# Performance work log

Measured on AMD Instinct MI355X. Metric: run time of the kernel, lower is better.

Reference implementation:

```python
import jax, jax.numpy as jnp
import numpy as np

B, T, D = 2, 2048, 1024
H, K = 16, 64  # num_heads, key_size (value_size == key_size)


def setup_inputs() -> dict:
    key = jax.random.key(0)
    ks = jax.random.split(key, 9)
    # xavier-uniform-ish scale for square-ish projections
    def xavier(k, shape):
        fan_in, fan_out = shape[0], shape[1]
        lim = jnp.sqrt(6.0 / (fan_in + fan_out))
        return jax.random.uniform(k, shape, jnp.float32, -lim, lim)
    return {
        "x_q": jax.random.normal(ks[0], (B, T, D), jnp.float32),
        "Wq": xavier(ks[1], (D, H * K)),
        "bq": jnp.zeros((H * K,), jnp.float32),
        "Wk": xavier(ks[2], (D, H * K)),
        "bk": jnp.zeros((H * K,), jnp.float32),
        "Wv": xavier(ks[3], (D, H * K)),
        "bv": jnp.zeros((H * K,), jnp.float32),
        "Wo": xavier(ks[4], (H * K, D)),
        "bo": jnp.zeros((D,), jnp.float32),
    }


def reference(x_q, Wq, bq, Wk, bk, Wv, bv, Wo, bo):
    # self-attention: x_k = x_v = x_q
    q = (x_q @ Wq + bq).reshape(B, T, H, K)
    k = (x_q @ Wk + bk).reshape(B, T, H, K)
    v = (x_q @ Wv + bv).reshape(B, T, H, K)
    # dense_dot_product_attention, mask=None
    logits = jnp.einsum('bqhd,bkhd->bhqk', q, k) / jnp.sqrt(jnp.asarray(K, k.dtype))
    attn_w = jax.nn.softmax(logits, axis=-1)  # [B,H,Tq,Tk]
    attn = jnp.einsum('bhqk,bkhd->bqhd', attn_w, v).reshape(B, T, H * K)
    out = attn @ Wo + bo  # [B,T,D]
    return out
```

## Files before the change

### kernel.cpp

```cpp
#include <hip/hip_runtime.h>
#include <hip/hip_bf16.h>
#include <stdint.h>

#define B_  2
#define T_  2048
#define D_  1024
#define H_  16
#define KS  64
#define M_  (B_*T_)

typedef unsigned short u16;
typedef __bf16 bf16x8 __attribute__((ext_vector_type(8)));
typedef __bf16 bf16x4 __attribute__((ext_vector_type(4)));
typedef float  f32x4  __attribute__((ext_vector_type(4)));

#define AS1 __attribute__((address_space(1)))
#define AS3 __attribute__((address_space(3)))

__device__ inline u16 f2bf(float x){
  union { float f; uint32_t u; } v; v.f = x;
  uint32_t r = (v.u + 0x7fffu + ((v.u >> 16) & 1u)) >> 16;
  return (u16)r;
}

__device__ inline void gl_lds16(const u16* g, u16* l){
  __builtin_amdgcn_global_load_lds((AS1 void*)(const_cast<u16*>(g)),
                                   (AS3 void*)l, 16, 0, 0);
}

__global__ __launch_bounds__(256) void k_cvt_x(const float* __restrict__ x,
                                               u16* __restrict__ xb){
  int i = blockIdx.x * 256 + threadIdx.x;
  float4 v = ((const float4*)x)[i];
  ushort4 o;
  o.x = f2bf(v.x); o.y = f2bf(v.y); o.z = f2bf(v.z); o.w = f2bf(v.w);
  ((ushort4*)xb)[i] = o;
}

__global__ __launch_bounds__(256) void k_tconv_w(const float* __restrict__ W0,
                                                 const float* __restrict__ W1,
                                                 const float* __restrict__ W2,
                                                 const float* __restrict__ W3,
                                                 u16* __restrict__ out){
  const float* W = (blockIdx.z==0)?W0:(blockIdx.z==1)?W1:(blockIdx.z==2)?W2:W3;
  u16* o = out + (size_t)blockIdx.z * 1024 * 1024;
  __shared__ float tile[32][33];
  int tx = threadIdx.x, ty = threadIdx.y;
  int kb = blockIdx.y * 32, nb = blockIdx.x * 32;
  for(int i=0;i<4;i++) tile[ty+8*i][tx] = W[(size_t)(kb+ty+8*i)*1024 + nb+tx];
  __syncthreads();
  for(int i=0;i<4;i++){
    int n = nb + ty + 8*i;
    o[(size_t)n*1024 + kb + tx] = f2bf(tile[tx][ty+8*i]);
  }
}

__global__ __launch_bounds__(256) void k_gemm_qkv(const u16* __restrict__ xb,
                                                  const u16* __restrict__ wt,
                                                  const float* __restrict__ bq,
                                                  const float* __restrict__ bk,
                                                  const float* __restrict__ bv,
                                                  u16* __restrict__ qkv){
  int widx = blockIdx.x >> 3;
  int n0   = (blockIdx.x & 7) * 128;
  int m0   = blockIdx.y * 128;
  const u16* BT = wt + (size_t)widx * (1024*1024);
  const float* bias = (widx==0)?bq:(widx==1)?bk:bv;
  u16* out = qkv + (size_t)widx * (4*1024*1024);
  float oscale = (widx==0) ? 0.125f * 1.44269504088896f : 1.0f;

  __shared__ u16 Asm[128*64];
  __shared__ u16 Bsm[128*64];
  int t = threadIdx.x;
  int lane = t & 63, w = t >> 6, wm = w >> 1, wn = w & 1;
  int l15 = lane & 15, l4 = lane >> 4;
  f32x4 zero = {0.f,0.f,0.f,0.f};
  f32x4 acc[4][4];
  for(int i=0;i<4;i++) for(int j=0;j<4;j++) acc[i][j] = zero;
  int srow = t >> 3, schunk = t & 7;

  for(int kt=0; kt<16; ++kt){
    __syncthreads();
    int kb = kt * 64;
    for(int i=0;i<4;i++){
      int row = i*32 + srow;
      int gch = schunk ^ (row & 7);
      gl_lds16(xb + (size_t)(m0+row)*1024 + kb + gch*8, Asm + row*64 + schunk*8);
      gl_lds16(BT + (size_t)(n0+row)*1024 + kb + gch*8, Bsm + row*64 + schunk*8);
    }
    __syncthreads();
    for(int c=0;c<2;c++){
      bf16x8 af[4], bfr[4];
      for(int mt=0;mt<4;mt++){
        int row = wm*64 + mt*16 + l15;
        int idx = (row*64 + c*32 + l4*8) ^ ((row & 7) << 3);
        af[mt] = *(const bf16x8*)(Asm + idx);
      }
      for(int nt=0;nt<4;nt++){
        int row = wn*64 + nt*16 + l15;
        int idx = (row*64 + c*32 + l4*8) ^ ((row & 7) << 3);
        bfr[nt] = *(const bf16x8*)(Bsm + idx);
      }
      for(int mt=0;mt<4;mt++)
        for(int nt=0;nt<4;nt++)
          acc[mt][nt] = __builtin_amdgcn_mfma_f32_16x16x32_bf16(af[mt], bfr[nt], acc[mt][nt], 0,0,0);
    }
  }
  for(int nt=0;nt<4;nt++){
    int nbase = n0 + wn*64 + nt*16 + l15;
    float bv_ = bias[nbase];
    int h = nbase >> 6, kk = nbase & 63;
    for(int mt=0;mt<4;mt++){
      for(int r=0;r<4;r++){
        int m = m0 + wm*64 + mt*16 + l4*4 + r;
        int b = m >> 11, tt = m & 2047;
        out[(((size_t)(b*H_ + h)*T_ + tt) << 6) + kk] = f2bf((acc[mt][nt][r] + bv_) * oscale);
      }
    }
  }
}

__global__ __launch_bounds__(256) void k_tpose_v(const u16* __restrict__ V,
                                                 u16* __restrict__ VT){
  __shared__ u16 tile[64][65];
  int bh = blockIdx.y, tt = blockIdx.x;
  const u16* v = V + ((size_t)bh*T_ + (size_t)tt*64) * 64;
  u16* o = VT + (size_t)bh*64*T_ + (size_t)tt*64;
  int t = threadIdx.x;
  for(int i=0;i<2;i++){
    int r = i*32 + (t>>3); int c0 = (t&7)*8;
    bf16x8 d = *(const bf16x8*)(v + (size_t)r*64 + c0);
    for(int j=0;j<8;j++) tile[r][c0+j] = ((u16*)&d)[j];
  }
  __syncthreads();
  for(int i=0;i<2;i++){
    int d0 = i*32 + (t>>3); int c0 = (t&7)*8;
    union { u16 s[8]; uint4 q; } pk;
    for(int j=0;j<8;j++) pk.s[j] = tile[c0+j][d0];
    *(uint4*)(o + (size_t)d0*T_ + c0) = pk.q;
  }
}

__global__ __launch_bounds__(256) void k_attn(const u16* __restrict__ Q,
                                              const u16* __restrict__ Kg,
                                              const u16* __restrict__ VT,
                                              u16* __restrict__ attn_out){
  int bx = blockIdx.x;
  int qt = bx & 31, h = (bx >> 5) & 15, b = bx >> 9;
  int bh = b*H_ + h;
  const u16* Qh = Q  + (size_t)bh * T_ * 64;
  const u16* Kh = Kg + (size_t)bh * T_ * 64;
  const u16* Vh = VT + (size_t)bh * 64 * T_;
  __shared__ u16 Ksm[2][64*64];
  __shared__ u16 Vsm[2][64*64];
  __shared__ u16 Psm[4][16*64];
  int t = threadIdx.x, lane = t & 63, w = t >> 6;
  int l15 = lane & 15, l4 = lane >> 4;

  bf16x8 qf[2];
  int qrow = qt*64 + w*16 + l15;
  for(int c=0;c<2;c++)
    qf[c] = *(const bf16x8*)(Qh + (size_t)qrow*64 + c*32 + l4*8);

  f32x4 zero = {0.f,0.f,0.f,0.f};
  f32x4 accT[4];
  for(int g=0;g<4;g++) accT[g] = zero;
  float m_r = -3.0e38f, l_r = 0.f;

  int srow = t >> 3, schunk = t & 7;

  for(int i=0;i<2;i++){
    int row = i*32 + srow;
    int gch = schunk ^ (row & 7);
    gl_lds16(Kh + (size_t)row*64 + gch*8,  &Ksm[0][row*64 + schunk*8]);
    gl_lds16(Vh + (size_t)row*T_ + gch*8,  &Vsm[0][row*64 + schunk*8]);
  }
  __syncthreads();

  int cur = 0;
  for(int tile=0; tile<32; ++tile){
    if(tile+1 < 32){
      int kvb = (tile+1)*64;
      for(int i=0;i<2;i++){
        int row = i*32 + srow;
        int gch = schunk ^ (row & 7);
        gl_lds16(Kh + (size_t)(kvb+row)*64 + gch*8, &Ksm[cur^1][row*64 + schunk*8]);
        gl_lds16(Vh + (size_t)row*T_ + kvb + gch*8, &Vsm[cur^1][row*64 + schunk*8]);
      }
    }

    f32x4 s[4];
    for(int g=0;g<4;g++) s[g] = zero;
    for(int c=0;c<2;c++){
      for(int g=0;g<4;g++){
        int row = g*16 + l15;
        int idx = (row*64 + c*32 + l4*8) ^ ((row & 7) << 3);
        bf16x8 kf = *(const bf16x8*)(&Ksm[cur][idx]);
        s[g] = __builtin_amdgcn_mfma_f32_16x16x32_bf16(kf, qf[c], s[g], 0,0,0);
      }
    }

    float pmax = s[0][0];
    for(int g=0;g<4;g++)
      for(int r=0;r<4;r++) pmax = fmaxf(pmax, s[g][r]);
    pmax = fmaxf(pmax, __shfl_xor(pmax, 16));
    pmax = fmaxf(pmax, __shfl_xor(pmax, 32));
    float mnew  = fmaxf(m_r, pmax);
    float alpha = __builtin_amdgcn_exp2f(m_r - mnew);
    m_r = mnew;
    float rs = 0.f;
    for(int g=0;g<4;g++)
      for(int r=0;r<4;r++){
        float e = __builtin_amdgcn_exp2f(s[g][r] - mnew);
        s[g][r] = e;
        rs += e;
      }
    rs += __shfl_xor(rs, 16);
    rs += __shfl_xor(rs, 32);
    l_r = l_r * alpha + rs;
    for(int g=0;g<4;g++){
      f32x4 a = accT[g];
      for(int r=0;r<4;r++) a[r] *= alpha;
      accT[g] = a;
    }

    for(int g=0;g<4;g++){
      bf16x4 pk;
      for(int r=0;r<4;r++) pk[r] = (__bf16)s[g][r];
      int idx = (l15*64 + g*16 + l4*4) ^ ((l15 & 7) << 3);
      *(bf16x4*)(&Psm[w][idx]) = pk;
    }

    for(int c=0;c<2;c++){
      int idx_p = (l15*64 + c*32 + l4*8) ^ ((l15 & 7) << 3);
      bf16x8 pf = *(const bf16x8*)(&Psm[w][idx_p]);
      for(int g=0;g<4;g++){
        int row = g*16 + l15;
        int idx = (row*64 + c*32 + l4*8) ^ ((row & 7) << 3);
        bf16x8 vf = *(const bf16x8*)(&Vsm[cur][idx]);
        accT[g] = __builtin_amdgcn_mfma_f32_16x16x32_bf16(vf, pf, accT[g], 0,0,0);
      }
    }

    __syncthreads();
    cur ^= 1;
  }

  float oinv = 1.0f / l_r;
  int m = b*T_ + qt*64 + w*16 + l15;
  for(int g=0;g<4;g++){
    bf16x4 pk;
    for(int r=0;r<4;r++) pk[r] = (__bf16)(accT[g][r] * oinv);
    *(bf16x4*)(attn_out + (size_t)m*1024 + h*64 + g*16 + l4*4) = pk;
  }
}

__global__ __launch_bounds__(256) void k_gemm_out(const u16* __restrict__ A,
                                                  const u16* __restrict__ BT,
                                                  const float* __restrict__ bias,
                                                  float* __restrict__ out){
  int n0 = blockIdx.x * 128;
  int m0 = blockIdx.y * 128;
  __shared__ u16 Asm[128*64];
  __shared__ u16 Bsm[128*64];
  int t = threadIdx.x;
  int lane = t & 63, w = t >> 6, wm = w >> 1, wn = w & 1;
  int l15 = lane & 15, l4 = lane >> 4;
  f32x4 zero = {0.f,0.f,0.f,0.f};
  f32x4 acc[4][4];
  for(int i=0;i<4;i++) for(int j=0;j<4;j++) acc[i][j] = zero;
  int srow = t >> 3, schunk = t & 7;

  for(int kt=0; kt<16; ++kt){
    __syncthreads();
    int kb = kt * 64;
    for(int i=0;i<4;i++){
      int row = i*32 + srow;
      int gch = schunk ^ (row & 7);
      gl_lds16(A  + (size_t)(m0+row)*1024 + kb + gch*8, Asm + row*64 + schunk*8);
      gl_lds16(BT + (size_t)(n0+row)*1024 + kb + gch*8, Bsm + row*64 + schunk*8);
    }
    __syncthreads();
    for(int c=0;c<2;c++){
      bf16x8 af[4], bfr[4];
      for(int mt=0;mt<4;mt++){
        int row = wm*64 + mt*16 + l15;
        int idx = (row*64 + c*32 + l4*8) ^ ((row & 7) << 3);
        af[mt] = *(const bf16x8*)(Asm + idx);
      }
      for(int nt=0;nt<4;nt++){
        int row = wn*64 + nt*16 + l15;
        int idx = (row*64 + c*32 + l4*8) ^ ((row & 7) << 3);
        bfr[nt] = *(const bf16x8*)(Bsm + idx);
      }
      for(int mt=0;mt<4;mt++)
        for(int nt=0;nt<4;nt++)
          acc[mt][nt] = __builtin_amdgcn_mfma_f32_16x16x32_bf16(af[mt], bfr[nt], acc[mt][nt], 0,0,0);
    }
  }
  for(int nt=0;nt<4;nt++){
    int nbase = n0 + wn*64 + nt*16 + l15;
    float bv_ = bias[nbase];
    for(int mt=0;mt<4;mt++){
      for(int r=0;r<4;r++){
        int m = m0 + wm*64 + mt*16 + l4*4 + r;
        out[(size_t)m*1024 + nbase] = acc[mt][nt][r] + bv_;
      }
    }
  }
}

extern "C" void kernel_launch(void* const* d_in, const int* in_sizes, int n_in,
                              void* d_out, int out_size, void* d_ws, size_t ws_size,
                              hipStream_t stream){
  const float* x  = (const float*)d_in[0];
  const float* Wq = (const float*)d_in[1];
  const float* bq = (const float*)d_in[2];
  const float* Wk = (const float*)d_in[3];
  const float* bk = (const float*)d_in[4];
  const float* Wv = (const float*)d_in[5];
  const float* bv = (const float*)d_in[6];
  const float* Wo = (const float*)d_in[7];
  const float* bo = (const float*)d_in[8];
  float* out = (float*)d_out;
  char* ws = (char*)d_ws;

  u16* xb  = (u16*)(ws);
  u16* wt  = (u16*)(ws + (8u  << 20));
  u16* qkv = (u16*)(ws + (16u << 20));
  u16* vt  = (u16*)(ws + (40u << 20));
  u16* at  = (u16*)(ws + (48u << 20));

  k_cvt_x   <<<4096, 256, 0, stream>>>(x, xb);
  k_tconv_w <<<dim3(32,32,4), dim3(32,8), 0, stream>>>(Wq, Wk, Wv, Wo, wt);
  k_gemm_qkv<<<dim3(24,32), 256, 0, stream>>>(xb, wt, bq, bk, bv, qkv);
  k_tpose_v <<<dim3(32,32), 256, 0, stream>>>(qkv + (size_t)8*1024*1024, vt);
  k_attn    <<<1024, 256, 0, stream>>>(qkv, qkv + (size_t)4*1024*1024, vt, at);
  k_gemm_out<<<dim3(8,32), 256, 0, stream>>>(at, wt + (size_t)3*1024*1024, bo, out);
}
```

Measured before the change: 228.3 us.

## Load V directly to registers, lazily rescale softmax, raise MFMA priority, shrink out-GEMM tile

The attention kernel now reads V fragments straight from global memory into registers each tile instead of staging them through double-buffered shared memory. It also skips the online-softmax rescale unless the running max grows by more than a threshold, and raises wave priority around the MFMA blocks. The output GEMM tile drops from 128x128 to 64x128, doubling the grid for better CU occupancy. Direct V loads are issued in the same iteration they are used, so their latency may be exposed, and the lazy rescale risks exp overflow if logits are large.

```diff
diff --git a/kernel.cpp b/kernel.cpp
--- a/kernel.cpp
+++ b/kernel.cpp
@@ -152,7 +152,6 @@
   const u16* Kh = Kg + (size_t)bh * T_ * 64;
   const u16* Vh = VT + (size_t)bh * 64 * T_;
   __shared__ u16 Ksm[2][64*64];
-  __shared__ u16 Vsm[2][64*64];
   __shared__ u16 Psm[4][16*64];
   int t = threadIdx.x, lane = t & 63, w = t >> 6;
   int l15 = lane & 15, l4 = lane >> 4;
@@ -172,25 +171,31 @@
   for(int i=0;i<2;i++){
     int row = i*32 + srow;
     int gch = schunk ^ (row & 7);
-    gl_lds16(Kh + (size_t)row*64 + gch*8,  &Ksm[0][row*64 + schunk*8]);
-    gl_lds16(Vh + (size_t)row*T_ + gch*8,  &Vsm[0][row*64 + schunk*8]);
+    gl_lds16(Kh + (size_t)row*64 + gch*8, &Ksm[0][row*64 + schunk*8]);
   }
   __syncthreads();
 
   int cur = 0;
   for(int tile=0; tile<32; ++tile){
+    int kv0 = tile*64;
+
+    bf16x8 vf[2][4];
+    for(int c=0;c<2;c++)
+      for(int g=0;g<4;g++)
+        vf[c][g] = *(const bf16x8*)(Vh + (size_t)(g*16+l15)*T_ + kv0 + c*32 + l4*8);
+
     if(tile+1 < 32){
-      int kvb = (tile+1)*64;
+      int kvb = kv0 + 64;
       for(int i=0;i<2;i++){
         int row = i*32 + srow;
         int gch = schunk ^ (row & 7);
         gl_lds16(Kh + (size_t)(kvb+row)*64 + gch*8, &Ksm[cur^1][row*64 + schunk*8]);
-        gl_lds16(Vh + (size_t)row*T_ + kvb + gch*8, &Vsm[cur^1][row*64 + schunk*8]);
       }
     }
 
     f32x4 s[4];
     for(int g=0;g<4;g++) s[g] = zero;
+    __builtin_amdgcn_s_setprio(1);
     for(int c=0;c<2;c++){
       for(int g=0;g<4;g++){
         int row = g*16 + l15;
@@ -199,30 +204,34 @@
         s[g] = __builtin_amdgcn_mfma_f32_16x16x32_bf16(kf, qf[c], s[g], 0,0,0);
       }
     }
+    __builtin_amdgcn_s_setprio(0);
 
     float pmax = s[0][0];
     for(int g=0;g<4;g++)
       for(int r=0;r<4;r++) pmax = fmaxf(pmax, s[g][r]);
     pmax = fmaxf(pmax, __shfl_xor(pmax, 16));
     pmax = fmaxf(pmax, __shfl_xor(pmax, 32));
-    float mnew  = fmaxf(m_r, pmax);
-    float alpha = __builtin_amdgcn_exp2f(m_r - mnew);
-    m_r = mnew;
+    if(__any(pmax > m_r + 8.f)){
+      float mnew  = fmaxf(m_r, pmax);
+      float alpha = __builtin_amdgcn_exp2f(m_r - mnew);
+      m_r = mnew;
+      l_r *= alpha;
+      for(int g=0;g<4;g++){
+        f32x4 a = accT[g];
+        for(int r=0;r<4;r++) a[r] *= alpha;
+        accT[g] = a;
+      }
+    }
     float rs = 0.f;
     for(int g=0;g<4;g++)
       for(int r=0;r<4;r++){
-        float e = __builtin_amdgcn_exp2f(s[g][r] - mnew);
+        float e = __builtin_amdgcn_exp2f(s[g][r] - m_r);
         s[g][r] = e;
         rs += e;
       }
     rs += __shfl_xor(rs, 16);
     rs += __shfl_xor(rs, 32);
-    l_r = l_r * alpha + rs;
-    for(int g=0;g<4;g++){
-      f32x4 a = accT[g];
-      for(int r=0;r<4;r++) a[r] *= alpha;
-      accT[g] = a;
-    }
+    l_r += rs;
 
     for(int g=0;g<4;g++){
       bf16x4 pk;
@@ -231,16 +240,14 @@
       *(bf16x4*)(&Psm[w][idx]) = pk;
     }
 
+    __builtin_amdgcn_s_setprio(1);
     for(int c=0;c<2;c++){
       int idx_p = (l15*64 + c*32 + l4*8) ^ ((l15 & 7) << 3);
       bf16x8 pf = *(const bf16x8*)(&Psm[w][idx_p]);
-      for(int g=0;g<4;g++){
-        int row = g*16 + l15;
-        int idx = (row*64 + c*32 + l4*8) ^ ((row & 7) << 3);
-        bf16x8 vf = *(const bf16x8*)(&Vsm[cur][idx]);
-        accT[g] = __builtin_amdgcn_mfma_f32_16x16x32_bf16(vf, pf, accT[g], 0,0,0);
-      }
-    }
+      for(int g=0;g<4;g++)
+        accT[g] = __builtin_amdgcn_mfma_f32_16x16x32_bf16(vf[c][g], pf, accT[g], 0,0,0);
+    }
+    __builtin_amdgcn_s_setprio(0);
 
     __syncthreads();
     cur ^= 1;
@@ -260,31 +267,35 @@
                                                   const float* __restrict__ bias,
                                                   float* __restrict__ out){
   int n0 = blockIdx.x * 128;
-  int m0 = blockIdx.y * 128;
-  __shared__ u16 Asm[128*64];
+  int m0 = blockIdx.y * 64;
+  __shared__ u16 Asm[64*64];
   __shared__ u16 Bsm[128*64];
   int t = threadIdx.x;
   int lane = t & 63, w = t >> 6, wm = w >> 1, wn = w & 1;
   int l15 = lane & 15, l4 = lane >> 4;
   f32x4 zero = {0.f,0.f,0.f,0.f};
-  f32x4 acc[4][4];
-  for(int i=0;i<4;i++) for(int j=0;j<4;j++) acc[i][j] = zero;
+  f32x4 acc[2][4];
+  for(int i=0;i<2;i++) for(int j=0;j<4;j++) acc[i][j] = zero;
   int srow = t >> 3, schunk = t & 7;
 
   for(int kt=0; kt<16; ++kt){
     __syncthreads();
     int kb = kt * 64;
+    for(int i=0;i<2;i++){
+      int row = i*32 + srow;
+      int gch = schunk ^ (row & 7);
+      gl_lds16(A  + (size_t)(m0+row)*1024 + kb + gch*8, Asm + row*64 + schunk*8);
+    }
     for(int i=0;i<4;i++){
       int row = i*32 + srow;
       int gch = schunk ^ (row & 7);
-      gl_lds16(A  + (size_t)(m0+row)*1024 + kb + gch*8, Asm + row*64 + schunk*8);
       gl_lds16(BT + (size_t)(n0+row)*1024 + kb + gch*8, Bsm + row*64 + schunk*8);
     }
     __syncthreads();
     for(int c=0;c<2;c++){
-      bf16x8 af[4], bfr[4];
-      for(int mt=0;mt<4;mt++){
-        int row = wm*64 + mt*16 + l15;
+      bf16x8 af[2], bfr[4];
+      for(int mt=0;mt<2;mt++){
+        int row = wm*32 + mt*16 + l15;
         int idx = (row*64 + c*32 + l4*8) ^ ((row & 7) << 3);
         af[mt] = *(const bf16x8*)(Asm + idx);
       }
@@ -293,7 +304,7 @@
         int idx = (row*64 + c*32 + l4*8) ^ ((row & 7) << 3);
         bfr[nt] = *(const bf16x8*)(Bsm + idx);
       }
-      for(int mt=0;mt<4;mt++)
+      for(int mt=0;mt<2;mt++)
         for(int nt=0;nt<4;nt++)
           acc[mt][nt] = __builtin_amdgcn_mfma_f32_16x16x32_bf16(af[mt], bfr[nt], acc[mt][nt], 0,0,0);
     }
@@ -301,9 +312,9 @@
   for(int nt=0;nt<4;nt++){
     int nbase = n0 + wn*64 + nt*16 + l15;
     float bv_ = bias[nbase];
-    for(int mt=0;mt<4;mt++){
+    for(int mt=0;mt<2;mt++){
       for(int r=0;r<4;r++){
-        int m = m0 + wm*64 + mt*16 + l4*4 + r;
+        int m = m0 + wm*32 + mt*16 + l4*4 + r;
         out[(size_t)m*1024 + nbase] = acc[mt][nt][r] + bv_;
       }
     }
@@ -336,5 +347,5 @@
   k_gemm_qkv<<<dim3(24,32), 256, 0, stream>>>(xb, wt, bq, bk, bv, qkv);
   k_tpose_v <<<dim3(32,32), 256, 0, stream>>>(qkv + (size_t)8*1024*1024, vt);
   k_attn    <<<1024, 256, 0, stream>>>(qkv, qkv + (size_t)4*1024*1024, vt, at);
-  k_gemm_out<<<dim3(8,32), 256, 0, stream>>>(at, wt + (size_t)3*1024*1024, bo, out);
-}
+  k_gemm_out<<<dim3(8,64), 256, 0, stream>>>(at, wt + (size_t)3*1024*1024, bo, out);
+}
```

New measurement: 305.3 us. 1.34x slower.
